# Performance work log

Measured on AMD Instinct MI355X. Metric: run time of the kernel, lower is better.

## Reference

```python
import jax, jax.numpy as jnp
import numpy as np

DEPTH = 4
HIDDEN = 256
ATOM_FDIM = 143
BOND_FDIM = 14
N_ATOMS = 65536
N_BONDS = 131072
MAX_NB = 6
ATOMS_PER_MOL = 32


def setup_inputs() -> dict:
    key = jax.random.key(0)
    ks = jax.random.split(key, 12)
    s = 0.05  # weight init scale
    return {
        'fatoms': jax.random.uniform(ks[0], (N_ATOMS, ATOM_FDIM), dtype=jnp.float32),
        'fbonds': jax.random.uniform(ks[1], (N_BONDS, ATOM_FDIM + BOND_FDIM), dtype=jnp.float32),
        'agraph': jax.random.randint(ks[2], (N_ATOMS, MAX_NB), 0, N_BONDS, dtype=jnp.int32),
        'bgraph': jax.random.randint(ks[3], (N_BONDS, MAX_NB), 0, N_BONDS, dtype=jnp.int32),
        'atoms_per_mol': ATOMS_PER_MOL,
        'W_i': jax.random.normal(ks[4], (ATOM_FDIM + BOND_FDIM, HIDDEN), dtype=jnp.float32) * s,
        'W_h': jax.random.normal(ks[5], (HIDDEN, HIDDEN), dtype=jnp.float32) * s,
        'W_o_w': jax.random.normal(ks[6], (ATOM_FDIM + HIDDEN, HIDDEN), dtype=jnp.float32) * s,
        'W_o_b': jax.random.normal(ks[7], (HIDDEN,), dtype=jnp.float32) * s,
        'W_a': jax.random.normal(ks[8], (HIDDEN, HIDDEN), dtype=jnp.float32) * s,
        'W_b_w': jax.random.normal(ks[9], (HIDDEN, HIDDEN), dtype=jnp.float32) * s,
        'W_b_b': jax.random.normal(ks[10], (HIDDEN,), dtype=jnp.float32) * s,
        'W_ma1': jax.random.normal(ks[11], (HIDDEN, 1), dtype=jnp.float32) * s,
    }


def reference(fatoms, fbonds, agraph, bgraph, atoms_per_mol,
              W_i, W_h, W_o_w, W_o_b, W_a, W_b_w, W_b_b, W_ma1):
    act = jax.nn.relu  # activation == 'ReLU'; dropout == 0 (identity)

    binput = fbonds @ W_i                      # [E, H]
    message = act(binput)
    for _ in range(DEPTH - 1):
        nei = message[bgraph]                  # [E, max_nb, H] gather
        # message attention over incoming messages (softmax over neighbor axis)
        att = jax.nn.softmax(nei @ W_ma1, axis=1)  # [E, max_nb, 1]
        nei = (nei * att).sum(axis=1)          # [E, H]
        message = act(binput + nei @ W_h)

    nei_a = message[agraph].sum(axis=1)        # [N, H]
    ainput = jnp.concatenate([fatoms, nei_a], axis=1)
    atom_h = act(ainput @ W_o_w + W_o_b)       # [N, H]

    # per-molecule self-attention pooling; equal-size molecules -> batched
    A = atoms_per_mol
    B = atom_h.shape[0] // A
    h = atom_h.reshape(B, A, HIDDEN)           # [B, A, H]
    scores = jnp.einsum('bad,bcd->bac', h @ W_a, h)   # [B, A, A]
    att_w = jax.nn.softmax(scores, axis=-1)
    att_h = act(jnp.einsum('bac,bcd->bad', att_w, h) @ W_b_w + W_b_b)
    mol_vecs = (h + att_h).sum(axis=1) / A     # [B, H]
    return mol_vecs
```

## Files before the change

kernel.cpp:

```cpp
#include <hip/hip_runtime.h>

typedef unsigned short u16;
typedef __attribute__((ext_vector_type(8))) short short8;
typedef __attribute__((ext_vector_type(4))) float floatx4;

__device__ __forceinline__ float bf2f(u16 u) {
    return __uint_as_float(((unsigned int)u) << 16);
}
__device__ __forceinline__ u16 f2bf(float f) {
    unsigned int i = __float_as_uint(f);
    unsigned int r = i + 0x7FFFu + ((i >> 16) & 1u);
    return (u16)(r >> 16);
}
__device__ __forceinline__ unsigned int relu2(unsigned int x) {
    unsigned int m = (((x >> 15) & 1u) * 0x0000FFFFu) | ((x >> 31) * 0xFFFF0000u);
    return x & ~m;
}

typedef __attribute__((address_space(3))) void lds_void;
typedef const __attribute__((address_space(1))) void g_void;
__device__ __forceinline__ void async_copy16(const void* g, void* l) {
    __builtin_amdgcn_global_load_lds((g_void*)g, (lds_void*)l, 16, 0, 0);
}

__device__ __forceinline__ void acc_bf8(float* a8, uint4 u, float wj) {
    a8[0] += wj * __uint_as_float(u.x << 16);
    a8[1] += wj * __uint_as_float(u.x & 0xffff0000u);
    a8[2] += wj * __uint_as_float(u.y << 16);
    a8[3] += wj * __uint_as_float(u.y & 0xffff0000u);
    a8[4] += wj * __uint_as_float(u.z << 16);
    a8[5] += wj * __uint_as_float(u.z & 0xffff0000u);
    a8[6] += wj * __uint_as_float(u.w << 16);
    a8[7] += wj * __uint_as_float(u.w & 0xffff0000u);
}

#define MFMA16(a, b, c) __builtin_amdgcn_mfma_f32_16x16x32_bf16(a, b, c, 0, 0, 0)

#define E_BONDS 131072
#define N_ATOMS_C 65536
#define KPAD_I 160
#define KPAD_O 416
#define N_MOLS 2048

__global__ __launch_bounds__(256) void prep_fbonds(const float* __restrict__ fb, u16* __restrict__ out) {
    int idx = blockIdx.x * 256 + threadIdx.x;
    int row = idx / KPAD_I;
    int col = idx - row * KPAD_I;
    float v = (col < 157) ? fb[(size_t)row * 157 + col] : 0.f;
    out[idx] = f2bf(v);
}

__global__ __launch_bounds__(256) void prep_wt(const float* __restrict__ W, u16* __restrict__ Wt, int K, int Kpad) {
    int idx = blockIdx.x * 256 + threadIdx.x;
    int n = idx / Kpad;
    int k = idx - n * Kpad;
    float v = (k < K) ? W[(size_t)k * 256 + n] : 0.f;
    Wt[idx] = f2bf(v);
}

__global__ __launch_bounds__(256) void prep_wo(const float* __restrict__ W, u16* __restrict__ Wt) {
    int idx = blockIdx.x * 256 + threadIdx.x;
    int n = idx / KPAD_O;
    int k = idx - n * KPAD_O;
    float v = 0.f;
    if (k < 256)      v = W[(size_t)(143 + k) * 256 + n];
    else if (k < 399) v = W[(size_t)(k - 256) * 256 + n];
    Wt[idx] = f2bf(v);
}

template <int EPI, bool RELUA>
__global__ __launch_bounds__(512, 3) void gemm256(
    const u16* __restrict__ A, const u16* __restrict__ Bt,
    u16* __restrict__ out,
    const float* __restrict__ bias, const float* __restrict__ wma,
    float* __restrict__ tout, int K)
{
    __shared__ char ldsbuf[33792];
    u16* Al = (u16*)ldsbuf;
    u16* Bl = (u16*)(ldsbuf + 8192);

    const int tid = threadIdx.x;
    const int w = tid >> 6, lane = tid & 63;
    const int quad = lane >> 4, mr = lane & 15;
    const int m0 = blockIdx.x * 128;

    floatx4 acc[16] = {};

    const u16* Ag = A + (size_t)(m0 + (tid & 127)) * K + ((tid >> 7) << 3);

    for (int k0 = 0; k0 < K; k0 += 32) {
        if (RELUA) {
            uint4 x = *(const uint4*)(Ag + k0);
            x.x = relu2(x.x); x.y = relu2(x.y); x.z = relu2(x.z); x.w = relu2(x.w);
            *(uint4*)(Al + tid * 8) = x;
        } else {
            async_copy16(Ag + k0, Al + tid * 8);
        }
#pragma unroll
        for (int i = 0; i < 2; ++i) {
            int c = tid + i * 512;
            async_copy16(Bt + (size_t)(c & 255) * K + k0 + ((c >> 8) << 3), Bl + c * 8);
        }
        __syncthreads();

        short8 af = *(const short8*)(Al + quad * 1024 + (w * 16 + mr) * 8);
#pragma unroll
        for (int j = 0; j < 16; ++j) {
            short8 bf = *(const short8*)(Bl + quad * 2048 + (j * 16 + mr) * 8);
            acc[j] = MFMA16(af, bf, acc[j]);
        }
        __syncthreads();
    }

    u16* slice = (u16*)ldsbuf + w * 2112;
    const int lhalf = lane >> 5;
    const int lcol = (lane & 31) * 8;
    float wmal8[8];
    if (EPI == 1) {
#pragma unroll
        for (int e = 0; e < 8; ++e) wmal8[e] = wma[lcol + e];
    }
    float bl16[16];
    if (EPI == 3) {
#pragma unroll
        for (int j = 0; j < 16; ++j) bl16[j] = bias[j * 16 + mr];
    }

#pragma unroll
    for (int p = 0; p < 2; ++p) {
        if ((quad >> 1) == p) {
            int lr = (quad & 1) * 4;
#pragma unroll
            for (int j = 0; j < 16; ++j)
#pragma unroll
                for (int r = 0; r < 4; ++r) {
                    float v = acc[j][r];
                    if (EPI == 3) { v += bl16[j]; v = v > 0.f ? v : 0.f; }
                    slice[(lr + r) * 264 + j * 16 + mr] = f2bf(v);
                }
        }
        __syncthreads();
#pragma unroll
        for (int round = 0; round < 4; ++round) {
            int rowl = round * 2 + lhalf;
            int row = m0 + w * 16 + p * 8 + rowl;
            size_t off = (size_t)row * 256 + lcol;
            short8 pv = *(const short8*)(slice + rowl * 264 + lcol);
            if (EPI == 0 || EPI == 3) {
                *(short8*)(out + off) = pv;
            } else {
                *(short8*)(out + off) = pv;
                float pdot = 0.f;
#pragma unroll
                for (int e = 0; e < 8; ++e) {
                    u16 u = (u16)pv[e];
                    u = (u & 0x8000u) ? (u16)0 : u;
                    pdot += bf2f(u) * wmal8[e];
                }
                pdot += __shfl_xor(pdot, 1); pdot += __shfl_xor(pdot, 2);
                pdot += __shfl_xor(pdot, 4); pdot += __shfl_xor(pdot, 8);
                pdot += __shfl_xor(pdot, 16);
                if ((lane & 31) == 0) tout[row] = pdot;
            }
        }
        __syncthreads();
    }
}

template <int MODE>
__global__ __launch_bounds__(512, 6) void fused_gg(
    const u16* src, const u16* __restrict__ Bt, const int* __restrict__ graph,
    const float* __restrict__ t_in, const u16* __restrict__ binput,
    const float* __restrict__ fatoms, const float* __restrict__ bias,
    const float* __restrict__ wma, u16* __restrict__ outp, float* __restrict__ t_out)
{
    constexpr int MT = (MODE == 2) ? 32 : 64;
    constexpr int KK = (MODE == 2) ? 416 : 256;
    constexpr int KP = KK + 8;
    constexpr int MF = MT / 16;
    constexpr int LDSB = (MODE == 2) ? (32 * 424 * 2) : (32 * 268 * 4);

    __shared__ __align__(16) char ldsbuf[LDSB];
    u16* As = (u16*)ldsbuf;

    const int tid = threadIdx.x;
    const int w = tid >> 6, lane = tid & 63;
    const int quad = lane >> 4, mr = lane & 15;
    const int hw = tid >> 5, l32 = tid & 31;
    const int m0 = blockIdx.x * MT;

    for (int it = 0; it < MT / 16; ++it) {
        const int r = it * 16 + hw;
        const int e = m0 + r;
        const int* bg = graph + (size_t)e * 6;
        int2 b01 = *(const int2*)bg;
        int2 b23 = *(const int2*)(bg + 2);
        int2 b45 = *(const int2*)(bg + 4);
        int b[6] = {b01.x, b01.y, b23.x, b23.y, b45.x, b45.y};

        float wg[6];
        if (MODE != 2) {
            float s[6];
#pragma unroll
            for (int j = 0; j < 6; ++j) s[j] = t_in[b[j]];
            float mx = fmaxf(fmaxf(fmaxf(s[0], s[1]), fmaxf(s[2], s[3])), fmaxf(s[4], s[5]));
            float den = 0.f;
#pragma unroll
            for (int j = 0; j < 6; ++j) { wg[j] = __expf(s[j] - mx); den += wg[j]; }
            float inv = 1.f / den;
#pragma unroll
            for (int j = 0; j < 6; ++j) wg[j] *= inv;
        }

        float a8[8] = {};
#pragma unroll
        for (int j = 0; j < 6; ++j) {
            uint4 u = *(const uint4*)(src + (size_t)b[j] * 256 + l32 * 8);
            if (MODE == 1) { u.x = relu2(u.x); u.y = relu2(u.y); u.z = relu2(u.z); u.w = relu2(u.w); }
            acc_bf8(a8, u, (MODE == 2) ? 1.f : wg[j]);
        }
        short8 mv;
#pragma unroll
        for (int k = 0; k < 8; ++k) mv[k] = (short)f2bf(a8[k]);
        *(short8*)(As + r * KP + l32 * 8) = mv;

        if (MODE == 2) {
            const float* frow = fatoms + (size_t)e * 143;
#pragma unroll
            for (int i = 0; i < 5; ++i) {
                int c = l32 + i * 32;
                As[r * KP + 256 + c] = (c < 143) ? f2bf(frow[c]) : (u16)0;
            }
        }
    }
    __syncthreads();

    floatx4 acc[MF][2] = {};
    const u16* bp0 = Bt + (size_t)(w * 32 + mr) * KK + quad * 8;
    const u16* bp1 = bp0 + (size_t)16 * KK;
#pragma unroll 2
    for (int ks = 0; ks < KK / 32; ++ks) {
        const int k0 = ks * 32;
        short8 bf0 = *(const short8*)(bp0 + k0);
        short8 bf1 = *(const short8*)(bp1 + k0);
#pragma unroll
        for (int mf = 0; mf < MF; ++mf) {
            short8 af = *(const short8*)(As + (mf * 16 + mr) * KP + k0 + quad * 8);
            acc[mf][0] = MFMA16(af, bf0, acc[mf][0]);
            acc[mf][1] = MFMA16(af, bf1, acc[mf][1]);
        }
    }
    __syncthreads();

    if (MODE != 2) {
        float* Pf = (float*)ldsbuf;
        const int rrow = tid >> 4;
        const int rcol = (tid & 15) * 16;
        float wv[16];
#pragma unroll
        for (int e2 = 0; e2 < 16; ++e2) wv[e2] = wma[rcol + e2];

#pragma unroll
        for (int p = 0; p < 2; ++p) {
#pragma unroll
            for (int mi = 0; mi < 2; ++mi) {
#pragma unroll
                for (int jj = 0; jj < 2; ++jj)
#pragma unroll
                    for (int r = 0; r < 4; ++r)
                        Pf[(mi * 16 + quad * 4 + r) * 268 + (w * 2 + jj) * 16 + mr] = acc[p * 2 + mi][jj][r];
            }
            __syncthreads();
            const int grow = m0 + p * 32 + rrow;
            const u16* brow = binput + (size_t)grow * 256 + rcol;
            uint4 bu0 = *(const uint4*)brow;
            uint4 bu1 = *(const uint4*)(brow + 8);
            float bv[16] = {
                __uint_as_float(bu0.x << 16), __uint_as_float(bu0.x & 0xffff0000u),
                __uint_as_float(bu0.y << 16), __uint_as_float(bu0.y & 0xffff0000u),
                __uint_as_float(bu0.z << 16), __uint_as_float(bu0.z & 0xffff0000u),
                __uint_as_float(bu0.w << 16), __uint_as_float(bu0.w & 0xffff0000u),
                __uint_as_float(bu1.x << 16), __uint_as_float(bu1.x & 0xffff0000u),
                __uint_as_float(bu1.y << 16), __uint_as_float(bu1.y & 0xffff0000u),
                __uint_as_float(bu1.z << 16), __uint_as_float(bu1.z & 0xffff0000u),
                __uint_as_float(bu1.w << 16), __uint_as_float(bu1.w & 0xffff0000u)};
            const float* prow = Pf + rrow * 268 + rcol;
            float pdot = 0.f;
            short8 o0, o1;
#pragma unroll
            for (int e2 = 0; e2 < 16; ++e2) {
                float v = prow[e2] + bv[e2];
                v = v > 0.f ? v : 0.f;
                u16 q = f2bf(v);
                if (e2 < 8) o0[e2] = (short)q; else o1[e2 - 8] = (short)q;
                pdot += bf2f(q) * wv[e2];
            }
            size_t off = (size_t)grow * 256 + rcol;
            *(short8*)(outp + off) = o0;
            *(short8*)(outp + off + 8) = o1;
            pdot += __shfl_xor(pdot, 1); pdot += __shfl_xor(pdot, 2);
            pdot += __shfl_xor(pdot, 4); pdot += __shfl_xor(pdot, 8);
            if ((lane & 15) == 0) t_out[grow] = pdot;
            __syncthreads();
        }
    } else {
        u16* Pu = (u16*)ldsbuf;
        float bl0 = bias[(w * 2 + 0) * 16 + mr];
        float bl1 = bias[(w * 2 + 1) * 16 + mr];
#pragma unroll
        for (int mf = 0; mf < MF; ++mf)
#pragma unroll
            for (int r = 0; r < 4; ++r) {
                float v0 = acc[mf][0][r] + bl0; v0 = v0 > 0.f ? v0 : 0.f;
                float v1 = acc[mf][1][r] + bl1; v1 = v1 > 0.f ? v1 : 0.f;
                Pu[(mf * 16 + quad * 4 + r) * 264 + (w * 2 + 0) * 16 + mr] = f2bf(v0);
                Pu[(mf * 16 + quad * 4 + r) * 264 + (w * 2 + 1) * 16 + mr] = f2bf(v1);
            }
        __syncthreads();
        const int rrow = tid >> 4;
        const int rcol = (tid & 15) * 16;
        size_t off = (size_t)(m0 + rrow) * 256 + rcol;
        short8 v0 = *(const short8*)(Pu + rrow * 264 + rcol);
        short8 v1 = *(const short8*)(Pu + rrow * 264 + rcol + 8);
        *(short8*)(outp + off) = v0;
        *(short8*)(outp + off + 8) = v1;
    }
}

#define HSTR 260
__global__ __launch_bounds__(256) void mol_attn(const u16* __restrict__ atomh, const u16* __restrict__ hWg,
                                                u16* __restrict__ z) {
    __shared__ float hs[32 * HSTR];
    __shared__ float P[32 * 33];
    const int t = threadIdx.x;
    const int b = blockIdx.x;
    const u16* hbase = atomh + (size_t)b * 32 * 256;
    for (int e0 = t * 4; e0 < 8192; e0 += 1024) {
        int row = e0 >> 8, col = e0 & 255;
        ushort4 u = *(const ushort4*)(hbase + e0);
        floatx4 v; v.x = bf2f(u.x); v.y = bf2f(u.y); v.z = bf2f(u.z); v.w = bf2f(u.w);
        *(floatx4*)&hs[row * HSTR + col] = v;
    }
    __syncthreads();

    {
        int c = t & 31, a0 = t >> 5;
        const u16* hWb = hWg + (size_t)b * 32 * 256;
        for (int r = 0; r < 4; ++r) {
            int a = a0 + r * 8;
            const u16* hwrow = hWb + a * 256;
            float s = 0.f;
            for (int d = 0; d < 256; d += 4) {
                ushort4 u = *(const ushort4*)(hwrow + d);
                const float* hp = &hs[c * HSTR + d];
                s += bf2f(u.x) * hp[0] + bf2f(u.y) * hp[1] + bf2f(u.z) * hp[2] + bf2f(u.w) * hp[3];
            }
            P[a * 33 + c] = s;
        }
    }
    __syncthreads();
    if (t < 32) {
        float* prow = &P[t * 33];
        float mx = prow[0];
        for (int i = 1; i < 32; ++i) mx = fmaxf(mx, prow[i]);
        float den = 0.f;
        for (int i = 0; i < 32; ++i) { float ev = __expf(prow[i] - mx); prow[i] = ev; den += ev; }
        float inv = 1.f / den;
        for (int i = 0; i < 32; ++i) prow[i] *= inv;
    }
    __syncthreads();

    {
        int a = t >> 3, q = t & 7;
        floatx4 acc8[8];
#pragma unroll
        for (int i = 0; i < 8; ++i) acc8[i] = (floatx4){0.f, 0.f, 0.f, 0.f};
        const float* prow = &P[a * 33];
        for (int cc = 0; cc < 32; ++cc) {
            float p = prow[cc];
            const float* hrow = &hs[cc * HSTR + q * 4];
#pragma unroll
            for (int i = 0; i < 8; ++i) {
                floatx4 hv = *(const floatx4*)(hrow + i * 32);
                acc8[i] += p * hv;
            }
        }
        u16* zrow = z + ((size_t)b * 32 + a) * 256 + q * 4;
#pragma unroll
        for (int i = 0; i < 8; ++i) {
            ushort4 o;
            o.x = f2bf(acc8[i].x); o.y = f2bf(acc8[i].y); o.z = f2bf(acc8[i].z); o.w = f2bf(acc8[i].w);
            *(ushort4*)(zrow + i * 32) = o;
        }
    }
}

__global__ __launch_bounds__(256) void final_reduce(const u16* __restrict__ atomh, const u16* __restrict__ atth,
                                                    float* __restrict__ out) {
    int idx = blockIdx.x * 256 + threadIdx.x;
    int b = idx >> 8, d = idx & 255;
    const u16* ph = atomh + ((size_t)b * 32) * 256 + d;
    const u16* pa = atth + ((size_t)b * 32) * 256 + d;
    float s = 0.f;
#pragma unroll 4
    for (int a = 0; a < 32; ++a) s += bf2f(ph[a * 256]) + bf2f(pa[a * 256]);
    out[idx] = s * 0.03125f;
}

#define O_FBP      ((size_t)0)
#define O_BINPUT   ((size_t)41943040)
#define O_MSGA     ((size_t)109051904)
#define O_MSGB     ((size_t)176160768)
#define O_W        ((size_t)243269632)
#define O_WTI      (O_W)
#define O_WTH      (O_W + 81920)
#define O_WTO      (O_W + 212992)
#define O_WTA      (O_W + 425984)
#define O_WTB      (O_W + 557056)
#define WS_NEED    ((size_t)243957760)

extern "C" void kernel_launch(void* const* d_in, const int* in_sizes, int n_in,
                              void* d_out, int out_size, void* d_ws, size_t ws_size,
                              hipStream_t stream) {
    const float* fatoms = (const float*)d_in[0];
    const float* fbonds = (const float*)d_in[1];
    const int*   agraph = (const int*)d_in[2];
    const int*   bgraph = (const int*)d_in[3];
    const float* W_i    = (const float*)d_in[5];
    const float* W_h    = (const float*)d_in[6];
    const float* W_o_w  = (const float*)d_in[7];
    const float* W_o_b  = (const float*)d_in[8];
    const float* W_a    = (const float*)d_in[9];
    const float* W_b_w  = (const float*)d_in[10];
    const float* W_b_b  = (const float*)d_in[11];
    const float* W_ma1  = (const float*)d_in[12];
    float* out = (float*)d_out;

    if (ws_size < WS_NEED) return;

    char* ws = (char*)d_ws;
    u16* fbp     = (u16*)(ws + O_FBP);
    u16* binput  = (u16*)(ws + O_BINPUT);
    u16* msgA    = (u16*)(ws + O_MSGA);
    u16* msgB    = (u16*)(ws + O_MSGB);
    u16* wti     = (u16*)(ws + O_WTI);
    u16* wth     = (u16*)(ws + O_WTH);
    u16* wto     = (u16*)(ws + O_WTO);
    u16* wta     = (u16*)(ws + O_WTA);
    u16* wtb     = (u16*)(ws + O_WTB);
    u16* atomh   = (u16*)(ws + O_FBP);
    u16* hW      = (u16*)(ws + O_BINPUT);
    u16* zbuf    = (u16*)(ws + O_BINPUT + 33554432);
    u16* atth    = (u16*)(ws + O_MSGA);
    float* tA = (float*)d_out;
    float* tB = tA + E_BONDS;

    prep_fbonds<<<81920, 256, 0, stream>>>(fbonds, fbp);
    prep_wt<<<160, 256, 0, stream>>>(W_i, wti, 157, KPAD_I);
    prep_wt<<<256, 256, 0, stream>>>(W_h, wth, 256, 256);
    prep_wo<<<416, 256, 0, stream>>>(W_o_w, wto);
    prep_wt<<<256, 256, 0, stream>>>(W_a, wta, 256, 256);
    prep_wt<<<256, 256, 0, stream>>>(W_b_w, wtb, 256, 256);

    gemm256<1, false><<<1024, 512, 0, stream>>>(fbp, wti, binput, nullptr, W_ma1, tA, KPAD_I);

    fused_gg<1><<<E_BONDS / 64, 512, 0, stream>>>(binput, wth, bgraph, tA, binput, nullptr, nullptr, W_ma1, msgA, tB);
    fused_gg<0><<<E_BONDS / 64, 512, 0, stream>>>(msgA,   wth, bgraph, tB, binput, nullptr, nullptr, W_ma1, msgB, tA);
    fused_gg<0><<<E_BONDS / 64, 512, 0, stream>>>(msgB,   wth, bgraph, tA, binput, nullptr, nullptr, W_ma1, msgA, tB);

    fused_gg<2><<<N_ATOMS_C / 32, 512, 0, stream>>>(msgA, wto, agraph, nullptr, nullptr, fatoms, W_o_b, nullptr, atomh, nullptr);

    gemm256<0, false><<<512, 512, 0, stream>>>(atomh, wta, hW, nullptr, nullptr, nullptr, 256);
    mol_attn<<<N_MOLS, 256, 0, stream>>>(atomh, hW, zbuf);
    gemm256<3, false><<<512, 512, 0, stream>>>(zbuf, wtb, atth, W_b_b, nullptr, nullptr, 256);

    final_reduce<<<N_MOLS, 256, 0, stream>>>(atomh, atth, out);
}
```

Baseline: 684.4 us.

## Fuse fbonds bf16 conversion into first GEMM and shrink fused_gg blocks to 256 threads

```diff
diff --git a/kernel.cpp b/kernel.cpp
--- a/kernel.cpp
+++ b/kernel.cpp
@@ -42,14 +42,6 @@
 #define KPAD_O 416
 #define N_MOLS 2048
 
-__global__ __launch_bounds__(256) void prep_fbonds(const float* __restrict__ fb, u16* __restrict__ out) {
-    int idx = blockIdx.x * 256 + threadIdx.x;
-    int row = idx / KPAD_I;
-    int col = idx - row * KPAD_I;
-    float v = (col < 157) ? fb[(size_t)row * 157 + col] : 0.f;
-    out[idx] = f2bf(v);
-}
-
 __global__ __launch_bounds__(256) void prep_wt(const float* __restrict__ W, u16* __restrict__ Wt, int K, int Kpad) {
     int idx = blockIdx.x * 256 + threadIdx.x;
     int n = idx / Kpad;
@@ -68,12 +60,12 @@
     Wt[idx] = f2bf(v);
 }
 
-template <int EPI, bool RELUA>
+template <int EPI, bool RELUA, bool F32A>
 __global__ __launch_bounds__(512, 3) void gemm256(
     const u16* __restrict__ A, const u16* __restrict__ Bt,
     u16* __restrict__ out,
     const float* __restrict__ bias, const float* __restrict__ wma,
-    float* __restrict__ tout, int K)
+    float* __restrict__ tout, int K, const float* __restrict__ Af32)
 {
     __shared__ char ldsbuf[33792];
     u16* Al = (u16*)ldsbuf;
@@ -86,10 +78,21 @@
 
     floatx4 acc[16] = {};
 
-    const u16* Ag = A + (size_t)(m0 + (tid & 127)) * K + ((tid >> 7) << 3);
+    const u16* Ag = F32A ? nullptr : (A + (size_t)(m0 + (tid & 127)) * K + ((tid >> 7) << 3));
+    const float* Af = F32A ? (Af32 + (size_t)(m0 + (tid & 127)) * 157) : nullptr;
 
     for (int k0 = 0; k0 < K; k0 += 32) {
-        if (RELUA) {
+        if (F32A) {
+            const int cb = k0 + ((tid >> 7) << 3);
+            short8 xv;
+#pragma unroll
+            for (int e = 0; e < 8; ++e) {
+                int c = cb + e;
+                float v = (c < 157) ? Af[c] : 0.f;
+                xv[e] = (short)f2bf(v);
+            }
+            *(short8*)(Al + tid * 8) = xv;
+        } else if (RELUA) {
             uint4 x = *(const uint4*)(Ag + k0);
             x.x = relu2(x.x); x.y = relu2(x.y); x.z = relu2(x.z); x.w = relu2(x.w);
             *(uint4*)(Al + tid * 8) = x;
@@ -168,17 +171,17 @@
 }
 
 template <int MODE>
-__global__ __launch_bounds__(512, 6) void fused_gg(
+__global__ __launch_bounds__(256, 6) void fused_gg(
     const u16* src, const u16* __restrict__ Bt, const int* __restrict__ graph,
     const float* __restrict__ t_in, const u16* __restrict__ binput,
     const float* __restrict__ fatoms, const float* __restrict__ bias,
     const float* __restrict__ wma, u16* __restrict__ outp, float* __restrict__ t_out)
 {
-    constexpr int MT = (MODE == 2) ? 32 : 64;
+    constexpr int MT = 32;
     constexpr int KK = (MODE == 2) ? 416 : 256;
     constexpr int KP = KK + 8;
-    constexpr int MF = MT / 16;
-    constexpr int LDSB = (MODE == 2) ? (32 * 424 * 2) : (32 * 268 * 4);
+    constexpr int ABYT = MT * KP * 2;
+    constexpr int LDSB = (MODE == 2) ? ABYT : (ABYT > 17152 ? ABYT : 17152);
 
     __shared__ __align__(16) char ldsbuf[LDSB];
     u16* As = (u16*)ldsbuf;
@@ -189,8 +192,9 @@
     const int hw = tid >> 5, l32 = tid & 31;
     const int m0 = blockIdx.x * MT;
 
-    for (int it = 0; it < MT / 16; ++it) {
-        const int r = it * 16 + hw;
+#pragma unroll
+    for (int it = 0; it < 4; ++it) {
+        const int r = it * 8 + hw;
         const int e = m0 + r;
         const int* bg = graph + (size_t)e * 6;
         int2 b01 = *(const int2*)bg;
@@ -235,26 +239,29 @@
     }
     __syncthreads();
 
-    floatx4 acc[MF][2] = {};
-    const u16* bp0 = Bt + (size_t)(w * 32 + mr) * KK + quad * 8;
-    const u16* bp1 = bp0 + (size_t)16 * KK;
+    floatx4 acc[2][4] = {};
+    const u16* bp = Bt + (size_t)(w * 64 + mr) * KK + quad * 8;
 #pragma unroll 2
     for (int ks = 0; ks < KK / 32; ++ks) {
         const int k0 = ks * 32;
-        short8 bf0 = *(const short8*)(bp0 + k0);
-        short8 bf1 = *(const short8*)(bp1 + k0);
-#pragma unroll
-        for (int mf = 0; mf < MF; ++mf) {
+        short8 bf0 = *(const short8*)(bp + k0);
+        short8 bf1 = *(const short8*)(bp + (size_t)16 * KK + k0);
+        short8 bf2 = *(const short8*)(bp + (size_t)32 * KK + k0);
+        short8 bf3 = *(const short8*)(bp + (size_t)48 * KK + k0);
+#pragma unroll
+        for (int mf = 0; mf < 2; ++mf) {
             short8 af = *(const short8*)(As + (mf * 16 + mr) * KP + k0 + quad * 8);
             acc[mf][0] = MFMA16(af, bf0, acc[mf][0]);
             acc[mf][1] = MFMA16(af, bf1, acc[mf][1]);
+            acc[mf][2] = MFMA16(af, bf2, acc[mf][2]);
+            acc[mf][3] = MFMA16(af, bf3, acc[mf][3]);
         }
     }
     __syncthreads();
 
     if (MODE != 2) {
         float* Pf = (float*)ldsbuf;
-        const int rrow = tid >> 4;
+        const int rr = tid >> 4;
         const int rcol = (tid & 15) * 16;
         float wv[16];
 #pragma unroll
@@ -263,15 +270,12 @@
 #pragma unroll
         for (int p = 0; p < 2; ++p) {
 #pragma unroll
-            for (int mi = 0; mi < 2; ++mi) {
-#pragma unroll
-                for (int jj = 0; jj < 2; ++jj)
-#pragma unroll
-                    for (int r = 0; r < 4; ++r)
-                        Pf[(mi * 16 + quad * 4 + r) * 268 + (w * 2 + jj) * 16 + mr] = acc[p * 2 + mi][jj][r];
-            }
+            for (int jj = 0; jj < 4; ++jj)
+#pragma unroll
+                for (int r = 0; r < 4; ++r)
+                    Pf[(quad * 4 + r) * 268 + (w * 4 + jj) * 16 + mr] = acc[p][jj][r];
             __syncthreads();
-            const int grow = m0 + p * 32 + rrow;
+            const int grow = m0 + p * 16 + rr;
             const u16* brow = binput + (size_t)grow * 256 + rcol;
             uint4 bu0 = *(const uint4*)brow;
             uint4 bu1 = *(const uint4*)(brow + 8);
@@ -284,7 +288,7 @@
                 __uint_as_float(bu1.y << 16), __uint_as_float(bu1.y & 0xffff0000u),
                 __uint_as_float(bu1.z << 16), __uint_as_float(bu1.z & 0xffff0000u),
                 __uint_as_float(bu1.w << 16), __uint_as_float(bu1.w & 0xffff0000u)};
-            const float* prow = Pf + rrow * 268 + rcol;
+            const float* prow = Pf + rr * 268 + rcol;
             float pdot = 0.f;
             short8 o0, o1;
 #pragma unroll
@@ -305,25 +309,28 @@
         }
     } else {
         u16* Pu = (u16*)ldsbuf;
-        float bl0 = bias[(w * 2 + 0) * 16 + mr];
-        float bl1 = bias[(w * 2 + 1) * 16 + mr];
-#pragma unroll
-        for (int mf = 0; mf < MF; ++mf)
-#pragma unroll
-            for (int r = 0; r < 4; ++r) {
-                float v0 = acc[mf][0][r] + bl0; v0 = v0 > 0.f ? v0 : 0.f;
-                float v1 = acc[mf][1][r] + bl1; v1 = v1 > 0.f ? v1 : 0.f;
-                Pu[(mf * 16 + quad * 4 + r) * 264 + (w * 2 + 0) * 16 + mr] = f2bf(v0);
-                Pu[(mf * 16 + quad * 4 + r) * 264 + (w * 2 + 1) * 16 + mr] = f2bf(v1);
-            }
+        float bl[4];
+#pragma unroll
+        for (int jj = 0; jj < 4; ++jj) bl[jj] = bias[(w * 4 + jj) * 16 + mr];
+#pragma unroll
+        for (int mf = 0; mf < 2; ++mf)
+#pragma unroll
+            for (int jj = 0; jj < 4; ++jj)
+#pragma unroll
+                for (int r = 0; r < 4; ++r) {
+                    float v = acc[mf][jj][r] + bl[jj];
+                    v = v > 0.f ? v : 0.f;
+                    Pu[(mf * 16 + quad * 4 + r) * 264 + (w * 4 + jj) * 16 + mr] = f2bf(v);
+                }
         __syncthreads();
-        const int rrow = tid >> 4;
-        const int rcol = (tid & 15) * 16;
-        size_t off = (size_t)(m0 + rrow) * 256 + rcol;
-        short8 v0 = *(const short8*)(Pu + rrow * 264 + rcol);
-        short8 v1 = *(const short8*)(Pu + rrow * 264 + rcol + 8);
-        *(short8*)(outp + off) = v0;
-        *(short8*)(outp + off + 8) = v1;
+#pragma unroll
+        for (int rr2 = 0; rr2 < 2; ++rr2) {
+            int row = rr2 * 16 + (tid >> 4);
+            int rcol = (tid & 15) * 16;
+            size_t off = (size_t)(m0 + row) * 256 + rcol;
+            *(short8*)(outp + off) = *(const short8*)(Pu + row * 264 + rcol);
+            *(short8*)(outp + off + 8) = *(const short8*)(Pu + row * 264 + rcol + 8);
+        }
     }
 }
 
@@ -439,7 +446,6 @@
     if (ws_size < WS_NEED) return;
 
     char* ws = (char*)d_ws;
-    u16* fbp     = (u16*)(ws + O_FBP);
     u16* binput  = (u16*)(ws + O_BINPUT);
     u16* msgA    = (u16*)(ws + O_MSGA);
     u16* msgB    = (u16*)(ws + O_MSGB);
@@ -455,24 +461,23 @@
     float* tA = (float*)d_out;
     float* tB = tA + E_BONDS;
 
-    prep_fbonds<<<81920, 256, 0, stream>>>(fbonds, fbp);
     prep_wt<<<160, 256, 0, stream>>>(W_i, wti, 157, KPAD_I);
     prep_wt<<<256, 256, 0, stream>>>(W_h, wth, 256, 256);
     prep_wo<<<416, 256, 0, stream>>>(W_o_w, wto);
     prep_wt<<<256, 256, 0, stream>>>(W_a, wta, 256, 256);
     prep_wt<<<256, 256, 0, stream>>>(W_b_w, wtb, 256, 256);
 
-    gemm256<1, false><<<1024, 512, 0, stream>>>(fbp, wti, binput, nullptr, W_ma1, tA, KPAD_I);
-
-    fused_gg<1><<<E_BONDS / 64, 512, 0, stream>>>(binput, wth, bgraph, tA, binput, nullptr, nullptr, W_ma1, msgA, tB);
-    fused_gg<0><<<E_BONDS / 64, 512, 0, stream>>>(msgA,   wth, bgraph, tB, binput, nullptr, nullptr, W_ma1, msgB, tA);
-    fused_gg<0><<<E_BONDS / 64, 512, 0, stream>>>(msgB,   wth, bgraph, tA, binput, nullptr, nullptr, W_ma1, msgA, tB);
-
-    fused_gg<2><<<N_ATOMS_C / 32, 512, 0, stream>>>(msgA, wto, agraph, nullptr, nullptr, fatoms, W_o_b, nullptr, atomh, nullptr);
-
-    gemm256<0, false><<<512, 512, 0, stream>>>(atomh, wta, hW, nullptr, nullptr, nullptr, 256);
+    gemm256<1, false, true><<<1024, 512, 0, stream>>>(nullptr, wti, binput, nullptr, W_ma1, tA, KPAD_I, fbonds);
+
+    fused_gg<1><<<E_BONDS / 32, 256, 0, stream>>>(binput, wth, bgraph, tA, binput, nullptr, nullptr, W_ma1, msgA, tB);
+    fused_gg<0><<<E_BONDS / 32, 256, 0, stream>>>(msgA,   wth, bgraph, tB, binput, nullptr, nullptr, W_ma1, msgB, tA);
+    fused_gg<0><<<E_BONDS / 32, 256, 0, stream>>>(msgB,   wth, bgraph, tA, binput, nullptr, nullptr, W_ma1, msgA, tB);
+
+    fused_gg<2><<<N_ATOMS_C / 32, 256, 0, stream>>>(msgA, wto, agraph, nullptr, nullptr, fatoms, W_o_b, nullptr, atomh, nullptr);
+
+    gemm256<0, false, false><<<512, 512, 0, stream>>>(atomh, wta, hW, nullptr, nullptr, nullptr, 256, nullptr);
     mol_attn<<<N_MOLS, 256, 0, stream>>>(atomh, hW, zbuf);
-    gemm256<3, false><<<512, 512, 0, stream>>>(zbuf, wtb, atth, W_b_b, nullptr, nullptr, 256);
+    gemm256<3, false, false><<<512, 512, 0, stream>>>(zbuf, wtb, atth, W_b_b, nullptr, nullptr, 256, nullptr);
 
     final_reduce<<<N_MOLS, 256, 0, stream>>>(atomh, atth, out);
 }
```

New measurement: 747.9 us. 9.3% more time.

## Fuse fp32-to-bf16 fbonds conversion into first GEMM and use nontemporal stores

Applied to the files above, without the earlier changes.

```diff
diff --git a/kernel.cpp b/kernel.cpp
--- a/kernel.cpp
+++ b/kernel.cpp
@@ -3,6 +3,7 @@
 typedef unsigned short u16;
 typedef __attribute__((ext_vector_type(8))) short short8;
 typedef __attribute__((ext_vector_type(4))) float floatx4;
+typedef __attribute__((ext_vector_type(4))) unsigned int uintx4;
 
 __device__ __forceinline__ float bf2f(u16 u) {
     return __uint_as_float(((unsigned int)u) << 16);
@@ -42,14 +43,6 @@
 #define KPAD_O 416
 #define N_MOLS 2048
 
-__global__ __launch_bounds__(256) void prep_fbonds(const float* __restrict__ fb, u16* __restrict__ out) {
-    int idx = blockIdx.x * 256 + threadIdx.x;
-    int row = idx / KPAD_I;
-    int col = idx - row * KPAD_I;
-    float v = (col < 157) ? fb[(size_t)row * 157 + col] : 0.f;
-    out[idx] = f2bf(v);
-}
-
 __global__ __launch_bounds__(256) void prep_wt(const float* __restrict__ W, u16* __restrict__ Wt, int K, int Kpad) {
     int idx = blockIdx.x * 256 + threadIdx.x;
     int n = idx / Kpad;
@@ -68,12 +61,12 @@
     Wt[idx] = f2bf(v);
 }
 
-template <int EPI, bool RELUA>
+template <int EPI, bool RELUA, bool F32A>
 __global__ __launch_bounds__(512, 3) void gemm256(
     const u16* __restrict__ A, const u16* __restrict__ Bt,
     u16* __restrict__ out,
     const float* __restrict__ bias, const float* __restrict__ wma,
-    float* __restrict__ tout, int K)
+    float* __restrict__ tout, int K, const float* __restrict__ Af32)
 {
     __shared__ char ldsbuf[33792];
     u16* Al = (u16*)ldsbuf;
@@ -86,10 +79,21 @@
 
     floatx4 acc[16] = {};
 
-    const u16* Ag = A + (size_t)(m0 + (tid & 127)) * K + ((tid >> 7) << 3);
+    const u16* Ag = F32A ? nullptr : (A + (size_t)(m0 + (tid & 127)) * K + ((tid >> 7) << 3));
+    const float* Af = F32A ? (Af32 + (size_t)(m0 + (tid & 127)) * 157) : nullptr;
 
     for (int k0 = 0; k0 < K; k0 += 32) {
-        if (RELUA) {
+        if (F32A) {
+            const int cb = k0 + ((tid >> 7) << 3);
+            short8 xv;
+#pragma unroll
+            for (int e = 0; e < 8; ++e) {
+                int c = cb + e;
+                float v = (c < 157) ? Af[c] : 0.f;
+                xv[e] = (short)f2bf(v);
+            }
+            *(short8*)(Al + tid * 8) = xv;
+        } else if (RELUA) {
             uint4 x = *(const uint4*)(Ag + k0);
             x.x = relu2(x.x); x.y = relu2(x.y); x.z = relu2(x.z); x.w = relu2(x.w);
             *(uint4*)(Al + tid * 8) = x;
@@ -229,7 +233,8 @@
 #pragma unroll
             for (int i = 0; i < 5; ++i) {
                 int c = l32 + i * 32;
-                As[r * KP + 256 + c] = (c < 143) ? f2bf(frow[c]) : (u16)0;
+                float fv = (c < 143) ? __builtin_nontemporal_load(frow + c) : 0.f;
+                As[r * KP + 256 + c] = (c < 143) ? f2bf(fv) : (u16)0;
             }
         }
     }
@@ -273,8 +278,8 @@
             __syncthreads();
             const int grow = m0 + p * 32 + rrow;
             const u16* brow = binput + (size_t)grow * 256 + rcol;
-            uint4 bu0 = *(const uint4*)brow;
-            uint4 bu1 = *(const uint4*)(brow + 8);
+            uintx4 bu0 = __builtin_nontemporal_load((const uintx4*)brow);
+            uintx4 bu1 = __builtin_nontemporal_load((const uintx4*)(brow + 8));
             float bv[16] = {
                 __uint_as_float(bu0.x << 16), __uint_as_float(bu0.x & 0xffff0000u),
                 __uint_as_float(bu0.y << 16), __uint_as_float(bu0.y & 0xffff0000u),
@@ -296,11 +301,11 @@
                 pdot += bf2f(q) * wv[e2];
             }
             size_t off = (size_t)grow * 256 + rcol;
-            *(short8*)(outp + off) = o0;
-            *(short8*)(outp + off + 8) = o1;
+            __builtin_nontemporal_store(o0, (short8*)(outp + off));
+            __builtin_nontemporal_store(o1, (short8*)(outp + off + 8));
             pdot += __shfl_xor(pdot, 1); pdot += __shfl_xor(pdot, 2);
             pdot += __shfl_xor(pdot, 4); pdot += __shfl_xor(pdot, 8);
-            if ((lane & 15) == 0) t_out[grow] = pdot;
+            if ((lane & 15) == 0) __builtin_nontemporal_store(pdot, t_out + grow);
             __syncthreads();
         }
     } else {
@@ -322,8 +327,8 @@
         size_t off = (size_t)(m0 + rrow) * 256 + rcol;
         short8 v0 = *(const short8*)(Pu + rrow * 264 + rcol);
         short8 v1 = *(const short8*)(Pu + rrow * 264 + rcol + 8);
-        *(short8*)(outp + off) = v0;
-        *(short8*)(outp + off + 8) = v1;
+        __builtin_nontemporal_store(v0, (short8*)(outp + off));
+        __builtin_nontemporal_store(v1, (short8*)(outp + off + 8));
     }
 }
 
@@ -439,7 +444,6 @@
     if (ws_size < WS_NEED) return;
 
     char* ws = (char*)d_ws;
-    u16* fbp     = (u16*)(ws + O_FBP);
     u16* binput  = (u16*)(ws + O_BINPUT);
     u16* msgA    = (u16*)(ws + O_MSGA);
     u16* msgB    = (u16*)(ws + O_MSGB);
@@ -455,14 +459,13 @@
     float* tA = (float*)d_out;
     float* tB = tA + E_BONDS;
 
-    prep_fbonds<<<81920, 256, 0, stream>>>(fbonds, fbp);
     prep_wt<<<160, 256, 0, stream>>>(W_i, wti, 157, KPAD_I);
     prep_wt<<<256, 256, 0, stream>>>(W_h, wth, 256, 256);
     prep_wo<<<416, 256, 0, stream>>>(W_o_w, wto);
     prep_wt<<<256, 256, 0, stream>>>(W_a, wta, 256, 256);
     prep_wt<<<256, 256, 0, stream>>>(W_b_w, wtb, 256, 256);
 
-    gemm256<1, false><<<1024, 512, 0, stream>>>(fbp, wti, binput, nullptr, W_ma1, tA, KPAD_I);
+    gemm256<1, false, true><<<1024, 512, 0, stream>>>(nullptr, wti, binput, nullptr, W_ma1, tA, KPAD_I, fbonds);
 
     fused_gg<1><<<E_BONDS / 64, 512, 0, stream>>>(binput, wth, bgraph, tA, binput, nullptr, nullptr, W_ma1, msgA, tB);
     fused_gg<0><<<E_BONDS / 64, 512, 0, stream>>>(msgA,   wth, bgraph, tB, binput, nullptr, nullptr, W_ma1, msgB, tA);
@@ -470,9 +473,9 @@
 
     fused_gg<2><<<N_ATOMS_C / 32, 512, 0, stream>>>(msgA, wto, agraph, nullptr, nullptr, fatoms, W_o_b, nullptr, atomh, nullptr);
 
-    gemm256<0, false><<<512, 512, 0, stream>>>(atomh, wta, hW, nullptr, nullptr, nullptr, 256);
+    gemm256<0, false, false><<<512, 512, 0, stream>>>(atomh, wta, hW, nullptr, nullptr, nullptr, 256, nullptr);
     mol_attn<<<N_MOLS, 256, 0, stream>>>(atomh, hW, zbuf);
-    gemm256<3, false><<<512, 512, 0, stream>>>(zbuf, wtb, atth, W_b_b, nullptr, nullptr, 256);
+    gemm256<3, false, false><<<512, 512, 0, stream>>>(zbuf, wtb, atth, W_b_b, nullptr, nullptr, 256, nullptr);
 
     final_reduce<<<N_MOLS, 256, 0, stream>>>(atomh, atth, out);
 }
```

After: 729.9 us. +6.6%, slower.
